# Performance work log

Hardware: AMD Instinct MI355X
Metric: run time of the kernel (lower is better)

## Reference

```python
import jax, jax.numpy as jnp
import numpy as np

D = 768  # embedding_size

def setup_inputs() -> dict:
    key = jax.random.key(0)
    k1, k2, k3, k4 = jax.random.split(key, 4)
    B, S = 256, 512
    embeddings = jax.random.normal(k1, (B, S, D), dtype=jnp.float32)
    # nn.Linear(768, 1, bias=False).weight -> store as vector [D]
    w_att = jax.random.normal(k2, (D,), dtype=jnp.float32) * (1.0 / np.sqrt(D))
    # nn.Linear(768, 1, bias=True)
    w_pred = jax.random.normal(k3, (D,), dtype=jnp.float32) * (1.0 / np.sqrt(D))
    b_pred = jax.random.normal(k4, (), dtype=jnp.float32) * (1.0 / np.sqrt(D))
    return {"embeddings": embeddings, "w_att": w_att, "w_pred": w_pred, "b_pred": b_pred}

def reference(embeddings, w_att, w_pred, b_pred):
    # Batched attention pooling (the torch code loops over batch; math is identical).
    # Dropout is inference-mode identity.
    scores = jnp.einsum('bsd,d->bs', embeddings, w_att)          # [B, S]
    attn = jax.nn.softmax(scores, axis=-1)                        # [B, S]
    pooled = jnp.einsum('bs,bsd->bd', attn, embeddings)           # [B, D]
    logits = jnp.einsum('bd,d->b', pooled, w_pred) + b_pred       # [B]
    return jax.nn.sigmoid(logits)                                 # [B]
```

## Files before the change

kernel.cpp:

```cpp
#include <hip/hip_runtime.h>
#include <math.h>

#define EMB_D 768
#define SEQ_S 512
#define BLOCK 1024
#define NWAVES (BLOCK / 64)
#define ROWS_PER_WAVE (SEQ_S / NWAVES)

__global__ __launch_bounds__(BLOCK, 1) void attn_pool_kernel(
    const float* __restrict__ emb,
    const float* __restrict__ w_att,
    const float* __restrict__ w_pred,
    const float* __restrict__ b_pred,
    float* __restrict__ out)
{
    __shared__ float s_score[SEQ_S];
    __shared__ float s_t[SEQ_S];
    __shared__ float s_red_a[NWAVES];
    __shared__ float s_red_b[NWAVES];

    const int b    = blockIdx.x;
    const int tid  = threadIdx.x;
    const int lane = tid & 63;
    const int wave = tid >> 6;

    const float4* wa4 = (const float4*)w_att;
    const float4* wp4 = (const float4*)w_pred;
    float4 wa[3], wp[3];
#pragma unroll
    for (int c = 0; c < 3; ++c) {
        wa[c] = wa4[lane + 64 * c];
        wp[c] = wp4[lane + 64 * c];
    }

    const float4* e4 = (const float4*)(emb + (size_t)b * SEQ_S * EMB_D);

#pragma unroll 1
    for (int r = 0; r < ROWS_PER_WAVE; ++r) {
        const int s = wave * ROWS_PER_WAVE + r;
        const float4* row = e4 + (size_t)s * (EMB_D / 4);
        float sa = 0.f, sp = 0.f;
#pragma unroll
        for (int c = 0; c < 3; ++c) {
            float4 v = row[lane + 64 * c];
            sa = fmaf(v.x, wa[c].x, sa);
            sa = fmaf(v.y, wa[c].y, sa);
            sa = fmaf(v.z, wa[c].z, sa);
            sa = fmaf(v.w, wa[c].w, sa);
            sp = fmaf(v.x, wp[c].x, sp);
            sp = fmaf(v.y, wp[c].y, sp);
            sp = fmaf(v.z, wp[c].z, sp);
            sp = fmaf(v.w, wp[c].w, sp);
        }
#pragma unroll
        for (int off = 32; off > 0; off >>= 1) {
            sa += __shfl_down(sa, off, 64);
            sp += __shfl_down(sp, off, 64);
        }
        if (lane == 0) {
            s_score[s] = sa;
            s_t[s]     = sp;
        }
    }
    __syncthreads();

    float score = -INFINITY, tval = 0.f;
    if (tid < SEQ_S) {
        score = s_score[tid];
        tval  = s_t[tid];
    }

    float m = score;
#pragma unroll
    for (int off = 1; off < 64; off <<= 1)
        m = fmaxf(m, __shfl_xor(m, off, 64));
    if (lane == 0) s_red_a[wave] = m;
    __syncthreads();
    if (tid == 0) {
        float mm = s_red_a[0];
#pragma unroll
        for (int w = 1; w < NWAVES; ++w) mm = fmaxf(mm, s_red_a[w]);
        s_red_a[0] = mm;
    }
    __syncthreads();
    m = s_red_a[0];
    __syncthreads();

    float e = (tid < SEQ_S) ? __expf(score - m) : 0.f;
    float se  = e;
    float set = e * tval;
#pragma unroll
    for (int off = 1; off < 64; off <<= 1) {
        se  += __shfl_xor(se, off, 64);
        set += __shfl_xor(set, off, 64);
    }
    if (lane == 0) {
        s_red_a[wave] = se;
        s_red_b[wave] = set;
    }
    __syncthreads();
    if (tid == 0) {
        float Z = 0.f, ET = 0.f;
#pragma unroll
        for (int w = 0; w < NWAVES; ++w) {
            Z  += s_red_a[w];
            ET += s_red_b[w];
        }
        float logit = ET / Z + b_pred[0];
        out[b] = 1.0f / (1.0f + __expf(-logit));
    }
}

extern "C" void kernel_launch(void* const* d_in, const int* in_sizes, int n_in,
                              void* d_out, int out_size, void* d_ws, size_t ws_size,
                              hipStream_t stream) {
    const float* emb    = (const float*)d_in[0];
    const float* w_att  = (const float*)d_in[1];
    const float* w_pred = (const float*)d_in[2];
    const float* b_pred = (const float*)d_in[3];
    float* out = (float*)d_out;

    const int B = in_sizes[0] / (SEQ_S * EMB_D);
    attn_pool_kernel<<<B, BLOCK, 0, stream>>>(emb, w_att, w_pred, b_pred, out);
}
```

Baseline: 522.8 us.

## Batch eight rows per wave with transposed butterfly reduction

Each wave now handles eight rows per iteration and issues twelve float4 loads at a time (two groups of four rows), so more memory requests are in flight per wave. The per-row 6-step shuffle reductions are replaced by a butterfly that splits the eight row sums across lane groups, which cuts the shuffle count per row. The cost is more registers per thread, and occupancy is already fixed at one 1024-thread block.

After: 527.2 us. Within noise of the previous version (+0.8%).

```diff
diff --git a/kernel.cpp b/kernel.cpp
--- a/kernel.cpp
+++ b/kernel.cpp
@@ -1,11 +1,13 @@
 #include <hip/hip_runtime.h>
 #include <math.h>
+
 
 #define EMB_D 768
 #define SEQ_S 512
 #define BLOCK 1024
 #define NWAVES (BLOCK / 64)
 #define ROWS_PER_WAVE (SEQ_S / NWAVES)
+#define RB 8
 
 __global__ __launch_bounds__(BLOCK, 1) void attn_pool_kernel(
     const float* __restrict__ emb,
@@ -35,31 +37,70 @@
 
     const float4* e4 = (const float4*)(emb + (size_t)b * SEQ_S * EMB_D);
 
+    const bool s0b = (lane & 1) != 0;
+    const bool s1b = (lane & 2) != 0;
+    const bool s2b = (lane & 4) != 0;
+
 #pragma unroll 1
-    for (int r = 0; r < ROWS_PER_WAVE; ++r) {
-        const int s = wave * ROWS_PER_WAVE + r;
-        const float4* row = e4 + (size_t)s * (EMB_D / 4);
-        float sa = 0.f, sp = 0.f;
+    for (int base = 0; base < ROWS_PER_WAVE; base += RB) {
+        const int s0 = wave * ROWS_PER_WAVE + base;
+        const float4* rp = e4 + (size_t)s0 * (EMB_D / 4) + lane;
+
+        float sa[RB], sp[RB];
 #pragma unroll
-        for (int c = 0; c < 3; ++c) {
-            float4 v = row[lane + 64 * c];
-            sa = fmaf(v.x, wa[c].x, sa);
-            sa = fmaf(v.y, wa[c].y, sa);
-            sa = fmaf(v.z, wa[c].z, sa);
-            sa = fmaf(v.w, wa[c].w, sa);
-            sp = fmaf(v.x, wp[c].x, sp);
-            sp = fmaf(v.y, wp[c].y, sp);
-            sp = fmaf(v.z, wp[c].z, sp);
-            sp = fmaf(v.w, wp[c].w, sp);
+        for (int r = 0; r < RB; ++r) { sa[r] = 0.f; sp[r] = 0.f; }
+
+#pragma unroll
+        for (int h = 0; h < 2; ++h) {
+            float4 v[4][3];
+#pragma unroll
+            for (int r = 0; r < 4; ++r)
+#pragma unroll
+                for (int c = 0; c < 3; ++c)
+                    v[r][c] = rp[(h * 4 + r) * (EMB_D / 4) + 64 * c];
+#pragma unroll
+            for (int r = 0; r < 4; ++r) {
+#pragma unroll
+                for (int c = 0; c < 3; ++c) {
+                    const int rr = h * 4 + r;
+                    sa[rr] = fmaf(v[r][c].x, wa[c].x, sa[rr]);
+                    sa[rr] = fmaf(v[r][c].y, wa[c].y, sa[rr]);
+                    sa[rr] = fmaf(v[r][c].z, wa[c].z, sa[rr]);
+                    sa[rr] = fmaf(v[r][c].w, wa[c].w, sa[rr]);
+                    sp[rr] = fmaf(v[r][c].x, wp[c].x, sp[rr]);
+                    sp[rr] = fmaf(v[r][c].y, wp[c].y, sp[rr]);
+                    sp[rr] = fmaf(v[r][c].z, wp[c].z, sp[rr]);
+                    sp[rr] = fmaf(v[r][c].w, wp[c].w, sp[rr]);
+                }
+            }
         }
+
+        float ua[4], up[4];
 #pragma unroll
-        for (int off = 32; off > 0; off >>= 1) {
-            sa += __shfl_down(sa, off, 64);
-            sp += __shfl_down(sp, off, 64);
+        for (int j = 0; j < 4; ++j) {
+            ua[j] = (s0b ? sa[2*j+1] : sa[2*j])
+                  + __shfl_xor(s0b ? sa[2*j] : sa[2*j+1], 1, 64);
+            up[j] = (s0b ? sp[2*j+1] : sp[2*j])
+                  + __shfl_xor(s0b ? sp[2*j] : sp[2*j+1], 1, 64);
         }
-        if (lane == 0) {
-            s_score[s] = sa;
-            s_t[s]     = sp;
+        float pa[2], pq[2];
+#pragma unroll
+        for (int j = 0; j < 2; ++j) {
+            pa[j] = (s1b ? ua[2*j+1] : ua[2*j])
+                  + __shfl_xor(s1b ? ua[2*j] : ua[2*j+1], 2, 64);
+            pq[j] = (s1b ? up[2*j+1] : up[2*j])
+                  + __shfl_xor(s1b ? up[2*j] : up[2*j+1], 2, 64);
+        }
+        float ra = (s2b ? pa[1] : pa[0]) + __shfl_xor(s2b ? pa[0] : pa[1], 4, 64);
+        float rt = (s2b ? pq[1] : pq[0]) + __shfl_xor(s2b ? pq[0] : pq[1], 4, 64);
+#pragma unroll
+        for (int off = 8; off < 64; off <<= 1) {
+            ra += __shfl_xor(ra, off, 64);
+            rt += __shfl_xor(rt, off, 64);
+        }
+        if (lane < RB) {
+            s_score[s0 + lane] = ra;
+            s_t[s0 + lane]     = rt;
         }
     }
     __syncthreads();
```
